# Performance work log

Measured on AMD Instinct MI355X. Metric: run time of the kernel, lower is better.

The kernel has to match this reference:

```python
import jax, jax.numpy as jnp
import numpy as np

B, N, F, P, E, T = 8, 10000, 8, 12, 160000, 64
C = 32  # A3TGCN2 out_channels fixed to 32 in the module


def setup_inputs() -> dict:
    key = jax.random.key(0)
    ks = jax.random.split(key, 20)
    x = jax.random.normal(ks[0], (B, N, F, P), jnp.float32)
    edge_index = jax.random.randint(ks[1], (2, E), 0, N, dtype=jnp.int64)
    edge_weight = jax.random.uniform(ks[2], (E,), jnp.float32)

    def g(k, shape):
        return jax.random.normal(k, shape, jnp.float32) * 0.05

    return dict(
        x=x, edge_index=edge_index, edge_weight=edge_weight,
        Wz=g(ks[3], (F, C)), bz=g(ks[4], (C,)),
        Wr=g(ks[5], (F, C)), br=g(ks[6], (C,)),
        Wh=g(ks[7], (F, C)), bh=g(ks[8], (C,)),
        Lz_w=g(ks[9], (2 * C, C)), Lz_b=g(ks[10], (C,)),
        Lr_w=g(ks[11], (2 * C, C)), Lr_b=g(ks[12], (C,)),
        Lh_w=g(ks[13], (2 * C, C)), Lh_b=g(ks[14], (C,)),
        att=g(ks[15], (P,)),
        lin1_w=g(ks[16], (C, P)), lin1_b=g(ks[17], (P,)),
        lin2_w=g(ks[18], (N, T)), lin2_b=g(ks[19], (T,)),
    )


def _gcn_norm(edge_index, edge_weight, n):
    # GCNConv default: add self-loops (weight 1) + symmetric normalization
    row, col = edge_index[0], edge_index[1]
    loop = jnp.arange(n)
    row = jnp.concatenate([row, loop])
    col = jnp.concatenate([col, loop])
    w = jnp.concatenate([edge_weight, jnp.ones((n,), edge_weight.dtype)])
    deg = jax.ops.segment_sum(w, col, num_segments=n)
    dis = jnp.where(deg > 0, jax.lax.rsqrt(jnp.where(deg > 0, deg, 1.0)), 0.0)
    return row, col, dis[row] * w * dis[col]


def _gcn_conv(X, W, b, row, col, norm, n):
    XW = X @ W                                   # [B,N,C]
    msg = XW[:, row, :] * norm[None, :, None]    # gather over source nodes
    out = jnp.zeros((X.shape[0], n, W.shape[1]), X.dtype).at[:, col, :].add(msg)
    return out + b


def reference(x, edge_index, edge_weight, Wz, bz, Wr, br, Wh, bh,
              Lz_w, Lz_b, Lr_w, Lr_b, Lh_w, Lh_b, att,
              lin1_w, lin1_b, lin2_w, lin2_b):
    b_, n, _, periods = x.shape
    row, col, norm = _gcn_norm(edge_index, edge_weight, n)
    probs = jax.nn.softmax(att)
    # A3TGCN2 passes H=None to the TGCN cell at every period -> hidden state
    # is zeros for every period (faithful to library implementation).
    H0 = jnp.zeros((b_, n, Lz_w.shape[1]), x.dtype)
    H_accum = jnp.zeros_like(H0)
    for p in range(periods):
        Xp = x[:, :, :, p]                       # [B,N,F]
        Z = jax.nn.sigmoid(
            jnp.concatenate([_gcn_conv(Xp, Wz, bz, row, col, norm, n), H0], axis=2) @ Lz_w + Lz_b)
        R = jax.nn.sigmoid(
            jnp.concatenate([_gcn_conv(Xp, Wr, br, row, col, norm, n), H0], axis=2) @ Lr_w + Lr_b)
        Ht = jnp.tanh(
            jnp.concatenate([_gcn_conv(Xp, Wh, bh, row, col, norm, n), H0 * R], axis=2) @ Lh_w + Lh_b)
        H = Z * H0 + (1.0 - Z) * Ht
        H_accum = H_accum + probs[p] * H
    h = jax.nn.relu(H_accum)                     # [B,N,32]
    h = h @ lin1_w + lin1_b                      # [B,N,P]
    h = jnp.swapaxes(h, 2, 1)                    # [B,P,N]
    h = h @ lin2_w + lin2_b                      # [B,P,T]
    return jnp.swapaxes(h, 2, 1)                 # [B,T,P]
```

## Files before the change

### kernel.cpp

```cpp
#include <hip/hip_runtime.h>
#include <stdint.h>

#define NN 10000
#define NB 8
#define NP 12
#define NT 64
#define NC 32
#define KFP 96
#define BCAP 96
#define FCN 100
#define FCH 100
#define XB 3750

__device__ __forceinline__ float bf_lo(unsigned u) { return __uint_as_float(u << 16); }
__device__ __forceinline__ float bf_hi(unsigned u) { return __uint_as_float(u & 0xffff0000u); }
__device__ __forceinline__ unsigned short f2bf(float f) {
    unsigned u = __float_as_uint(f);
    return (unsigned short)((u + 0x7fffu + ((u >> 16) & 1u)) >> 16);
}

__global__ __launch_bounds__(256) void k_build(
    const float* __restrict__ x,
    const int* __restrict__ rowp, const int* __restrict__ colp, const float* __restrict__ ew,
    const float* __restrict__ Wz, const float* __restrict__ bz,
    const float* __restrict__ Wh, const float* __restrict__ bh,
    const float* __restrict__ Lzw, const float* __restrict__ Lzb,
    const float* __restrict__ Lhw, const float* __restrict__ Lhb,
    const float* __restrict__ att, const float* __restrict__ l2b,
    float* __restrict__ sm, float* __restrict__ deg, int* __restrict__ count,
    uint2* __restrict__ bucket, unsigned short* __restrict__ xh,
    float* __restrict__ out, int E, int EB) {
    const int blk = blockIdx.x, tid = threadIdx.x;
    if (blk < XB) {
        const int s = blk * 256 + tid;
        const int n = s / 96, r = s - n * 96;
        const int b = r / 12, q = r - b * 12;
        const float* px = x + (size_t)b * 960000 + n * 96 + q * 8;
        const float4 f0 = *(const float4*)px;
        const float4 f1 = *(const float4*)(px + 4);
        unsigned u0 = (unsigned)f2bf(f0.x) | ((unsigned)f2bf(f0.y) << 16);
        unsigned u1 = (unsigned)f2bf(f0.z) | ((unsigned)f2bf(f0.w) << 16);
        unsigned u2 = (unsigned)f2bf(f1.x) | ((unsigned)f2bf(f1.y) << 16);
        unsigned u3 = (unsigned)f2bf(f1.z) | ((unsigned)f2bf(f1.w) << 16);
        *(uint4*)(xh + (size_t)s * 8) = make_uint4(u0, u1, u2, u3);
    } else if (blk < XB + EB) {
        const int e = (blk - XB) * 256 + tid;
        if (e < E) {
            const int c = colp[e];
            const float w = ew[e];
            atomicAdd(&deg[c], w);
            const int slot = atomicAdd(&count[c], 1);
            if (slot < BCAP) bucket[c * BCAP + slot] = make_uint2((unsigned)rowp[e], __float_as_uint(w));
        }
    } else if (blk == XB + EB) {
        const int t = tid, f = t >> 5, c = t & 31;
        float mz = 0.f, mh = 0.f;
        for (int j = 0; j < NC; ++j) {
            mz += Wz[f * NC + j] * Lzw[j * NC + c];
            mh += Wh[f * NC + j] * Lhw[j * NC + c];
        }
        sm[16 + t]  = mz;
        sm[272 + t] = mh;
        if (t < NC) {
            float cz = Lzb[t], ch = Lhb[t];
            for (int j = 0; j < NC; ++j) {
                cz += bz[j] * Lzw[j * NC + t];
                ch += bh[j] * Lhw[j * NC + t];
            }
            sm[528 + t] = cz;
            sm[560 + t] = ch;
        }
        if (t == 0) {
            float m = -1e30f;
            for (int p = 0; p < NP; ++p) m = fmaxf(m, att[p]);
            float e[NP]; float s = 0.f;
            for (int p = 0; p < NP; ++p) { e[p] = __expf(att[p] - m); s += e[p]; }
            for (int p = 0; p < NP; ++p) sm[p] = e[p] / s;
        }
    } else {
        for (int idx = tid; idx < NB * NT * NP; idx += 256) {
            const int t = (idx / 12) & 63;
            out[idx] = l2b[t];
        }
    }
}

__global__ __launch_bounds__(256) void k_main(
    const unsigned short* __restrict__ xh, const float* __restrict__ deg,
    const int* __restrict__ count, const uint2* __restrict__ bucket,
    const float* __restrict__ sm,
    const float* __restrict__ l1w, const float* __restrict__ l1b,
    float* __restrict__ h1t) {
    __shared__ float2 sMzh[256];
    __shared__ float2 sczh[32];
    __shared__ float  sprobs[12], sl1b[12];
    __shared__ float  sl1w[384];
    __shared__ float  sY[4][800];
    __shared__ float  sHA[4][264];
    __shared__ uint2  sE[4][64];

    const int tid = threadIdx.x;
    const int wv = tid >> 6, l = tid & 63;
    const int n = blockIdx.x * 4 + wv;

    sMzh[tid] = make_float2(sm[16 + tid], sm[272 + tid]);
    if (tid < 32) sczh[tid] = make_float2(sm[528 + tid], sm[560 + tid]);
    if (tid < 12) { sprobs[tid] = sm[tid]; sl1b[tid] = l1b[tid]; }
    for (int i = tid; i < 384; i += 256) sl1w[i] = l1w[i];
    __syncthreads();

    const char* xbase = (const char*)xh;
    const unsigned loff = (unsigned)l * 24u;
    const float dn = rsqrtf(deg[n] + 1.0f);
    float a[12];
    {
        const float sn = dn * dn;
        const char* p0 = xbase + ((unsigned)n * 1536u + loff);
        const uint2 u0 = *(const uint2*)p0;
        const uint2 u1 = *(const uint2*)(p0 + 8);
        const uint2 u2 = *(const uint2*)(p0 + 16);
        a[0] = bf_lo(u0.x) * sn; a[1]  = bf_hi(u0.x) * sn;
        a[2] = bf_lo(u0.y) * sn; a[3]  = bf_hi(u0.y) * sn;
        a[4] = bf_lo(u1.x) * sn; a[5]  = bf_hi(u1.x) * sn;
        a[6] = bf_lo(u1.y) * sn; a[7]  = bf_hi(u1.y) * sn;
        a[8] = bf_lo(u2.x) * sn; a[9]  = bf_hi(u2.x) * sn;
        a[10] = bf_lo(u2.y) * sn; a[11] = bf_hi(u2.y) * sn;
    }
    const int cnt = min(count[n], BCAP);
    const uint2* bk = bucket + n * BCAP;
    uint2* sEw = &sE[wv][0];
    for (int base = 0; base < cnt; base += 64) {
        const int m_ = min(64, cnt - base);
        if (l < m_) {
            const uint2 e = bk[base + l];
            const float w = __uint_as_float(e.y);
            const float d = deg[e.x];
            const float nrm = rsqrtf(d + 1.0f) * w * dn;
            sEw[l] = make_uint2(e.x * 1536u, __float_as_uint(nrm));
        }
        for (int q = 0; q < m_; ++q) {
            const uint2 e = sEw[q];
            const float w = __uint_as_float(e.y);
            const char* p = xbase + (e.x + loff);
            const uint2 u0 = *(const uint2*)p;
            const uint2 u1 = *(const uint2*)(p + 8);
            const uint2 u2 = *(const uint2*)(p + 16);
            a[0] = fmaf(bf_lo(u0.x), w, a[0]); a[1]  = fmaf(bf_hi(u0.x), w, a[1]);
            a[2] = fmaf(bf_lo(u0.y), w, a[2]); a[3]  = fmaf(bf_hi(u0.y), w, a[3]);
            a[4] = fmaf(bf_lo(u1.x), w, a[4]); a[5]  = fmaf(bf_hi(u1.x), w, a[5]);
            a[6] = fmaf(bf_lo(u1.y), w, a[6]); a[7]  = fmaf(bf_hi(u1.y), w, a[7]);
            a[8] = fmaf(bf_lo(u2.x), w, a[8]); a[9]  = fmaf(bf_hi(u2.x), w, a[9]);
            a[10] = fmaf(bf_lo(u2.y), w, a[10]); a[11] = fmaf(bf_hi(u2.y), w, a[11]);
        }
    }
    {
        float* yp = &sY[wv][(l >> 3) * 100 + (l & 7) * 12];
        *(float4*)yp       = make_float4(a[0], a[1], a[2], a[3]);
        *(float4*)(yp + 4) = make_float4(a[4], a[5], a[6], a[7]);
        *(float4*)(yp + 8) = make_float4(a[8], a[9], a[10], a[11]);
    }

    const int c = l & 31;
    float2 m8[8];
    #pragma unroll
    for (int f = 0; f < 8; ++f) m8[f] = sMzh[f * 32 + c];
    const float2 czh = sczh[c];
    float pr[12];
    #pragma unroll
    for (int p = 0; p < 12; ++p) pr[p] = sprobs[p];

    #pragma unroll
    for (int t4 = 0; t4 < 4; ++t4) {
        const int b = t4 * 2 + (l >> 5);
        const float* yb = &sY[wv][b * 100];
        float szv[12], shv[12];
        #pragma unroll
        for (int p = 0; p < 12; ++p) { szv[p] = czh.x; shv[p] = czh.y; }
        #pragma unroll
        for (int f = 0; f < 8; ++f) {
            const float4 y0 = *(const float4*)(yb + f * 12);
            const float4 y1 = *(const float4*)(yb + f * 12 + 4);
            const float4 y2 = *(const float4*)(yb + f * 12 + 8);
            const float mz = m8[f].x, mh = m8[f].y;
            szv[0] = fmaf(y0.x, mz, szv[0]); shv[0] = fmaf(y0.x, mh, shv[0]);
            szv[1] = fmaf(y0.y, mz, szv[1]); shv[1] = fmaf(y0.y, mh, shv[1]);
            szv[2] = fmaf(y0.z, mz, szv[2]); shv[2] = fmaf(y0.z, mh, shv[2]);
            szv[3] = fmaf(y0.w, mz, szv[3]); shv[3] = fmaf(y0.w, mh, shv[3]);
            szv[4] = fmaf(y1.x, mz, szv[4]); shv[4] = fmaf(y1.x, mh, shv[4]);
            szv[5] = fmaf(y1.y, mz, szv[5]); shv[5] = fmaf(y1.y, mh, shv[5]);
            szv[6] = fmaf(y1.z, mz, szv[6]); shv[6] = fmaf(y1.z, mh, shv[6]);
            szv[7] = fmaf(y1.w, mz, szv[7]); shv[7] = fmaf(y1.w, mh, shv[7]);
            szv[8] = fmaf(y2.x, mz, szv[8]); shv[8] = fmaf(y2.x, mh, shv[8]);
            szv[9] = fmaf(y2.y, mz, szv[9]); shv[9] = fmaf(y2.y, mh, shv[9]);
            szv[10] = fmaf(y2.z, mz, szv[10]); shv[10] = fmaf(y2.z, mh, shv[10]);
            szv[11] = fmaf(y2.w, mz, szv[11]); shv[11] = fmaf(y2.w, mh, shv[11]);
        }
        float hacc = 0.f;
        #pragma unroll
        for (int p = 0; p < 12; ++p) {
            const float ez = __expf(-szv[p]);
            const float omz = ez * __builtin_amdgcn_rcpf(1.f + ez);
            const float e2 = __expf(2.f * shv[p]);
            const float th = fmaf(-2.f, __builtin_amdgcn_rcpf(e2 + 1.f), 1.f);
            hacc = fmaf(pr[p], omz * th, hacc);
        }
        sHA[wv][b * 33 + c] = fmaxf(hacc, 0.f);
    }

    {
        const int r = l;
        const int bb = r / 12, p = r - bb * 12;
        float s = sl1b[p];
        #pragma unroll
        for (int cc = 0; cc < 32; ++cc) s = fmaf(sHA[wv][bb * 33 + cc], sl1w[cc * 12 + p], s);
        h1t[n * 96 + r] = s;
    }
    if (l < 32) {
        const int r = l + 64;
        const int bb = r / 12, p = r - bb * 12;
        float s = sl1b[p];
        #pragma unroll
        for (int cc = 0; cc < 32; ++cc) s = fmaf(sHA[wv][bb * 33 + cc], sl1w[cc * 12 + p], s);
        h1t[n * 96 + r] = s;
    }
}

__global__ __launch_bounds__(256) void k_final(const float* __restrict__ h1t, const float* __restrict__ W2,
                                               float* __restrict__ out) {
    __shared__ float sh1[48 * FCN];
    const int tid = threadIdx.x;
    const int chunk = blockIdx.x >> 1, h = blockIdx.x & 1;
    const int n0 = chunk * FCN;
    const int i0 = h * 48;

    for (int idx = tid; idx < 48 * FCN; idx += 256) {
        const int nn = idx / 48, i = idx - nn * 48;
        sh1[i * FCN + nn] = h1t[(n0 + nn) * 96 + i0 + i];
    }
    __syncthreads();

    const int t = tid & 63, w = tid >> 6;
    const float* sh = &sh1[w * 12 * FCN];
    float acc[12];
    #pragma unroll
    for (int j = 0; j < 12; ++j) acc[j] = 0.f;

    for (int nn = 0; nn < FCN; nn += 4) {
        const float w20 = W2[(n0 + nn + 0) * NT + t];
        const float w21 = W2[(n0 + nn + 1) * NT + t];
        const float w22 = W2[(n0 + nn + 2) * NT + t];
        const float w23 = W2[(n0 + nn + 3) * NT + t];
        #pragma unroll
        for (int j = 0; j < 12; ++j) {
            const float4 hv = *(const float4*)&sh[j * FCN + nn];
            acc[j] = fmaf(hv.x, w20, fmaf(hv.y, w21, fmaf(hv.z, w22, fmaf(hv.w, w23, acc[j]))));
        }
    }

    float* po = out + (h * 4 + w) * 768 + t * 12;
    #pragma unroll
    for (int j = 0; j < 12; ++j) atomicAdd(po + j, acc[j]);
}

extern "C" void kernel_launch(void* const* d_in, const int* in_sizes, int n_in,
                              void* d_out, int out_size, void* d_ws, size_t ws_size,
                              hipStream_t stream) {
    const float* x    = (const float*)d_in[0];
    const int*   eidx = (const int*)d_in[1];
    const float* ew   = (const float*)d_in[2];
    const float* Wz   = (const float*)d_in[3];
    const float* bz   = (const float*)d_in[4];
    const float* Wh   = (const float*)d_in[7];
    const float* bh   = (const float*)d_in[8];
    const float* Lzw  = (const float*)d_in[9];
    const float* Lzb  = (const float*)d_in[10];
    const float* Lhw  = (const float*)d_in[13];
    const float* Lhb  = (const float*)d_in[14];
    const float* att  = (const float*)d_in[15];
    const float* l1w  = (const float*)d_in[16];
    const float* l1b  = (const float*)d_in[17];
    const float* W2   = (const float*)d_in[18];
    const float* l2b  = (const float*)d_in[19];
    float* out = (float*)d_out;
    const int E = in_sizes[2];
    const int EB = (E + 255) / 256;

    float* deg    = (float*)d_ws;
    int*   count  = (int*)(deg + 10240);
    uint2* bucket = (uint2*)(count + 10240);
    float* sm     = (float*)(bucket + NN * BCAP);
    float* h1t    = sm + 1024;
    unsigned short* xh = (unsigned short*)(h1t + NN * 96);

    const int* rowp = eidx;
    const int* colp = eidx + E;

    hipMemsetAsync(d_ws, 0, 2 * 10240 * 4, stream);
    hipLaunchKernelGGL(k_build, dim3(XB + EB + 2), dim3(256), 0, stream,
                       x, rowp, colp, ew, Wz, bz, Wh, bh, Lzw, Lzb, Lhw, Lhb, att, l2b,
                       sm, deg, count, bucket, xh, out, E, EB);
    hipLaunchKernelGGL(k_main, dim3(NN / 4), dim3(256), 0, stream,
                       xh, deg, count, bucket, sm, l1w, l1b, h1t);
    hipLaunchKernelGGL(k_final, dim3(FCH * 2), dim3(256), 0, stream, h1t, W2, out);
}
```

Baseline: 128.2 us.

## Split build kernel, unroll edge gather by four, merge gate math into one reciprocal

```diff
diff --git a/kernel.cpp b/kernel.cpp
--- a/kernel.cpp
+++ b/kernel.cpp
@@ -19,40 +19,44 @@
     return (unsigned short)((u + 0x7fffu + ((u >> 16) & 1u)) >> 16);
 }
 
-__global__ __launch_bounds__(256) void k_build(
-    const float* __restrict__ x,
-    const int* __restrict__ rowp, const int* __restrict__ colp, const float* __restrict__ ew,
+__global__ __launch_bounds__(256) void k_xf(const float* __restrict__ x,
+                                            unsigned short* __restrict__ xh) {
+    const int s = blockIdx.x * 256 + threadIdx.x;
+    const int n = s / 96, r = s - n * 96;
+    const int b = r / 12, q = r - b * 12;
+    const float* px = x + (size_t)b * 960000 + n * 96 + q * 8;
+    const float4 f0 = *(const float4*)px;
+    const float4 f1 = *(const float4*)(px + 4);
+    unsigned u0 = (unsigned)f2bf(f0.x) | ((unsigned)f2bf(f0.y) << 16);
+    unsigned u1 = (unsigned)f2bf(f0.z) | ((unsigned)f2bf(f0.w) << 16);
+    unsigned u2 = (unsigned)f2bf(f1.x) | ((unsigned)f2bf(f1.y) << 16);
+    unsigned u3 = (unsigned)f2bf(f1.z) | ((unsigned)f2bf(f1.w) << 16);
+    *(uint4*)(xh + (size_t)s * 8) = make_uint4(u0, u1, u2, u3);
+}
+
+__global__ __launch_bounds__(256) void k_edge(const int* __restrict__ rowp, const int* __restrict__ colp,
+                                              const float* __restrict__ ew,
+                                              float* __restrict__ deg, int* __restrict__ count,
+                                              uint2* __restrict__ bucket, int E) {
+    const int e = blockIdx.x * 256 + threadIdx.x;
+    if (e < E) {
+        const int c = colp[e];
+        const float w = ew[e];
+        atomicAdd(&deg[c], w);
+        const int slot = atomicAdd(&count[c], 1);
+        if (slot < BCAP) bucket[c * BCAP + slot] = make_uint2((unsigned)rowp[e], __float_as_uint(w));
+    }
+}
+
+__global__ __launch_bounds__(256) void k_misc(
     const float* __restrict__ Wz, const float* __restrict__ bz,
     const float* __restrict__ Wh, const float* __restrict__ bh,
     const float* __restrict__ Lzw, const float* __restrict__ Lzb,
     const float* __restrict__ Lhw, const float* __restrict__ Lhb,
     const float* __restrict__ att, const float* __restrict__ l2b,
-    float* __restrict__ sm, float* __restrict__ deg, int* __restrict__ count,
-    uint2* __restrict__ bucket, unsigned short* __restrict__ xh,
-    float* __restrict__ out, int E, int EB) {
-    const int blk = blockIdx.x, tid = threadIdx.x;
-    if (blk < XB) {
-        const int s = blk * 256 + tid;
-        const int n = s / 96, r = s - n * 96;
-        const int b = r / 12, q = r - b * 12;
-        const float* px = x + (size_t)b * 960000 + n * 96 + q * 8;
-        const float4 f0 = *(const float4*)px;
-        const float4 f1 = *(const float4*)(px + 4);
-        unsigned u0 = (unsigned)f2bf(f0.x) | ((unsigned)f2bf(f0.y) << 16);
-        unsigned u1 = (unsigned)f2bf(f0.z) | ((unsigned)f2bf(f0.w) << 16);
-        unsigned u2 = (unsigned)f2bf(f1.x) | ((unsigned)f2bf(f1.y) << 16);
-        unsigned u3 = (unsigned)f2bf(f1.z) | ((unsigned)f2bf(f1.w) << 16);
-        *(uint4*)(xh + (size_t)s * 8) = make_uint4(u0, u1, u2, u3);
-    } else if (blk < XB + EB) {
-        const int e = (blk - XB) * 256 + tid;
-        if (e < E) {
-            const int c = colp[e];
-            const float w = ew[e];
-            atomicAdd(&deg[c], w);
-            const int slot = atomicAdd(&count[c], 1);
-            if (slot < BCAP) bucket[c * BCAP + slot] = make_uint2((unsigned)rowp[e], __float_as_uint(w));
-        }
-    } else if (blk == XB + EB) {
+    float* __restrict__ sm, float* __restrict__ out) {
+    const int tid = threadIdx.x;
+    if (blockIdx.x == 0) {
         const int t = tid, f = t >> 5, c = t & 31;
         float mz = 0.f, mh = 0.f;
         for (int j = 0; j < NC; ++j) {
@@ -84,6 +88,14 @@
         }
     }
 }
+
+#define ACC3(U0, U1, U2, W)                                                     \
+    a[0] = fmaf(bf_lo(U0.x), W, a[0]); a[1]  = fmaf(bf_hi(U0.x), W, a[1]);      \
+    a[2] = fmaf(bf_lo(U0.y), W, a[2]); a[3]  = fmaf(bf_hi(U0.y), W, a[3]);      \
+    a[4] = fmaf(bf_lo(U1.x), W, a[4]); a[5]  = fmaf(bf_hi(U1.x), W, a[5]);      \
+    a[6] = fmaf(bf_lo(U1.y), W, a[6]); a[7]  = fmaf(bf_hi(U1.y), W, a[7]);      \
+    a[8] = fmaf(bf_lo(U2.x), W, a[8]); a[9]  = fmaf(bf_hi(U2.x), W, a[9]);      \
+    a[10] = fmaf(bf_lo(U2.y), W, a[10]); a[11] = fmaf(bf_hi(U2.y), W, a[11])
 
 __global__ __launch_bounds__(256) void k_main(
     const unsigned short* __restrict__ xh, const float* __restrict__ deg,
@@ -131,26 +143,33 @@
     uint2* sEw = &sE[wv][0];
     for (int base = 0; base < cnt; base += 64) {
         const int m_ = min(64, cnt - base);
-        if (l < m_) {
-            const uint2 e = bk[base + l];
-            const float w = __uint_as_float(e.y);
-            const float d = deg[e.x];
-            const float nrm = rsqrtf(d + 1.0f) * w * dn;
-            sEw[l] = make_uint2(e.x * 1536u, __float_as_uint(nrm));
-        }
-        for (int q = 0; q < m_; ++q) {
-            const uint2 e = sEw[q];
-            const float w = __uint_as_float(e.y);
-            const char* p = xbase + (e.x + loff);
-            const uint2 u0 = *(const uint2*)p;
-            const uint2 u1 = *(const uint2*)(p + 8);
-            const uint2 u2 = *(const uint2*)(p + 16);
-            a[0] = fmaf(bf_lo(u0.x), w, a[0]); a[1]  = fmaf(bf_hi(u0.x), w, a[1]);
-            a[2] = fmaf(bf_lo(u0.y), w, a[2]); a[3]  = fmaf(bf_hi(u0.y), w, a[3]);
-            a[4] = fmaf(bf_lo(u1.x), w, a[4]); a[5]  = fmaf(bf_hi(u1.x), w, a[5]);
-            a[6] = fmaf(bf_lo(u1.y), w, a[6]); a[7]  = fmaf(bf_hi(u1.y), w, a[7]);
-            a[8] = fmaf(bf_lo(u2.x), w, a[8]); a[9]  = fmaf(bf_hi(u2.x), w, a[9]);
-            a[10] = fmaf(bf_lo(u2.y), w, a[10]); a[11] = fmaf(bf_hi(u2.y), w, a[11]);
+        const int m4 = (m_ + 3) & ~3;
+        {
+            uint2 ent = make_uint2(0u, 0u);
+            if (l < m_) {
+                const uint2 e = bk[base + l];
+                const float w = __uint_as_float(e.y);
+                const float nrm = rsqrtf(deg[e.x] + 1.0f) * w * dn;
+                ent = make_uint2(e.x * 1536u, __float_as_uint(nrm));
+            }
+            if (l < m4) sEw[l] = ent;
+        }
+        for (int q = 0; q < m4; q += 4) {
+            const uint2 e0 = sEw[q + 0], e1 = sEw[q + 1], e2 = sEw[q + 2], e3 = sEw[q + 3];
+            const char* pA = xbase + (e0.x + loff);
+            const char* pB = xbase + (e1.x + loff);
+            const char* pC = xbase + (e2.x + loff);
+            const char* pD = xbase + (e3.x + loff);
+            const uint2 A0 = *(const uint2*)pA, A1 = *(const uint2*)(pA + 8), A2 = *(const uint2*)(pA + 16);
+            const uint2 B0 = *(const uint2*)pB, B1 = *(const uint2*)(pB + 8), B2 = *(const uint2*)(pB + 16);
+            const uint2 C0 = *(const uint2*)pC, C1 = *(const uint2*)(pC + 8), C2 = *(const uint2*)(pC + 16);
+            const uint2 D0 = *(const uint2*)pD, D1 = *(const uint2*)(pD + 8), D2 = *(const uint2*)(pD + 16);
+            const float w0 = __uint_as_float(e0.y), w1 = __uint_as_float(e1.y);
+            const float w2 = __uint_as_float(e2.y), w3 = __uint_as_float(e3.y);
+            ACC3(A0, A1, A2, w0);
+            ACC3(B0, B1, B2, w1);
+            ACC3(C0, C1, C2, w2);
+            ACC3(D0, D1, D2, w3);
         }
     }
     {
@@ -198,11 +217,11 @@
         float hacc = 0.f;
         #pragma unroll
         for (int p = 0; p < 12; ++p) {
-            const float ez = __expf(-szv[p]);
-            const float omz = ez * __builtin_amdgcn_rcpf(1.f + ez);
-            const float e2 = __expf(2.f * shv[p]);
-            const float th = fmaf(-2.f, __builtin_amdgcn_rcpf(e2 + 1.f), 1.f);
-            hacc = fmaf(pr[p], omz * th, hacc);
+            const float u = __expf(-szv[p]);
+            const float v = __expf(2.f * shv[p]);
+            const float num = u * (v - 1.f);
+            const float den = fmaf(u, v, u) + (v + 1.f);
+            hacc = fmaf(pr[p] * num, __builtin_amdgcn_rcpf(den), hacc);
         }
         sHA[wv][b * 33 + c] = fmaxf(hacc, 0.f);
     }
@@ -296,9 +315,10 @@
     const int* colp = eidx + E;
 
     hipMemsetAsync(d_ws, 0, 2 * 10240 * 4, stream);
-    hipLaunchKernelGGL(k_build, dim3(XB + EB + 2), dim3(256), 0, stream,
-                       x, rowp, colp, ew, Wz, bz, Wh, bh, Lzw, Lzb, Lhw, Lhb, att, l2b,
-                       sm, deg, count, bucket, xh, out, E, EB);
+    hipLaunchKernelGGL(k_xf,   dim3(XB), dim3(256), 0, stream, x, xh);
+    hipLaunchKernelGGL(k_edge, dim3(EB), dim3(256), 0, stream, rowp, colp, ew, deg, count, bucket, E);
+    hipLaunchKernelGGL(k_misc, dim3(2), dim3(256), 0, stream,
+                       Wz, bz, Wh, bh, Lzw, Lzb, Lhw, Lhb, att, l2b, sm, out);
     hipLaunchKernelGGL(k_main, dim3(NN / 4), dim3(256), 0, stream,
                        xh, deg, count, bucket, sm, l1w, l1b, h1t);
     hipLaunchKernelGGL(k_final, dim3(FCH * 2), dim3(256), 0, stream, h1t, W2, out);
```

Result: slower. 132.6 us (+3.4%).
